# Performance work log

Hardware: AMD Instinct MI355X
Metric: run time of the kernel (lower is better)

## Reference

```python
import jax, jax.numpy as jnp
import numpy as np

NUM_HEADS = 16
NEG_INF = -9e15


def setup_inputs() -> dict:
    key = jax.random.key(0)
    k1, k2, k3 = jax.random.split(key, 3)
    B, S, D = 2, 2048, 1024
    # xavier-uniform-ish init scale for weights
    lim_qkv = float(np.sqrt(6.0 / (D + 3 * D)))
    lim_o = float(np.sqrt(6.0 / (D + D)))
    return {
        "x": jax.random.normal(k1, (B, S, D), dtype=jnp.float32),
        "w_qkv": jax.random.uniform(k2, (3 * D, D), minval=-lim_qkv, maxval=lim_qkv, dtype=jnp.float32),
        "b_qkv": jnp.zeros((3 * D,), dtype=jnp.float32),
        "w_o": jax.random.uniform(k3, (D, D), minval=-lim_o, maxval=lim_o, dtype=jnp.float32),
        "b_o": jnp.zeros((D,), dtype=jnp.float32),
    }


def reference(x, w_qkv, b_qkv, w_o, b_o):
    B, S, D = x.shape
    H = NUM_HEADS
    hd = D // H
    # qkv projection: [B,S,3D]
    qkv = x @ w_qkv.T + b_qkv
    # -> [B, H, S, 3*hd], then split
    qkv = qkv.reshape(B, S, H, 3 * hd).transpose(0, 2, 1, 3)
    q, k, v = jnp.split(qkv, 3, axis=-1)  # each [B,H,S,hd]
    scale = 1.0 / jnp.sqrt(jnp.asarray(hd, dtype=x.dtype))
    logits = jnp.einsum("bhqd,bhkd->bhqk", q, k) * scale
    attn = jax.nn.softmax(logits, axis=-1)
    vals = jnp.einsum("bhqk,bhkd->bhqd", attn, v)
    vals = vals.transpose(0, 2, 1, 3).reshape(B, S, D)
    return vals @ w_o.T + b_o
```

## Files before the change

### kernel.cpp

```cpp
#include <hip/hip_runtime.h>
#include <math.h>

#define NHEADS 16
#define HD 64

typedef __attribute__((ext_vector_type(8))) _Float16 half8;
typedef __attribute__((ext_vector_type(4))) _Float16 half4;
typedef __attribute__((ext_vector_type(4))) float f32x4;
typedef __attribute__((ext_vector_type(16))) float f32x16;
typedef __attribute__((ext_vector_type(4))) unsigned int u32x4;

__device__ inline void load_lds16(const void* g, void* l) {
    __builtin_amdgcn_global_load_lds(
        (const __attribute__((address_space(1))) unsigned int*)g,
        (__attribute__((address_space(3))) unsigned int*)l, 16, 0, 0);
}
__device__ inline void pl32swap(unsigned int& x, unsigned int& y) {
    asm volatile("v_permlane32_swap_b32 %0, %1" : "+v"(x), "+v"(y));
}

#define NX  4194304
#define NWQ 3145728
#define NWO 1048576
__global__ void cvt_all(const float* __restrict__ x, const float* __restrict__ wq,
                        const float* __restrict__ wo, _Float16* __restrict__ xf,
                        _Float16* __restrict__ wqf, _Float16* __restrict__ wof) {
    int i = (blockIdx.x * blockDim.x + threadIdx.x) * 8;
    const float* src; _Float16* dst; int off;
    if (i < NX)            { src = x;  dst = xf;  off = i; }
    else if (i < NX + NWQ) { src = wq; dst = wqf; off = i - NX; }
    else                   { src = wo; dst = wof; off = i - (NX + NWQ); }
    float4 a = *(const float4*)(src + off);
    float4 b = *(const float4*)(src + off + 4);
    half8 h;
    h[0] = (_Float16)a.x; h[1] = (_Float16)a.y; h[2] = (_Float16)a.z; h[3] = (_Float16)a.w;
    h[4] = (_Float16)b.x; h[5] = (_Float16)b.y; h[6] = (_Float16)b.z; h[7] = (_Float16)b.w;
    *(half8*)(dst + off) = h;
}

#define GEMM_SETUP(K, NTILE)                                                           \
    const int tid = threadIdx.x;                                                       \
    const int l = tid & 63, w = tid >> 6;                                              \
    const int wr = w >> 1, wc = w & 1;                                                 \
    const int nwg = gridDim.x * gridDim.y;                                             \
    const int bid = blockIdx.y * gridDim.x + blockIdx.x;                               \
    const int swz = (bid & 7) * (nwg >> 3) + (bid >> 3);                               \
    const int m0 = (swz / gridDim.x) * 128, n0 = (swz % gridDim.x) * (NTILE);          \
    const int srow = tid >> 2;                                                         \
    const int schunk = (tid & 3) ^ ((srow >> 1) & 3);                                  \
    const size_t gA0 = (size_t)(m0 + srow) * K + schunk * 8;                           \
    const size_t gA1 = gA0 + (size_t)64 * K;                                           \
    const size_t gB0 = (size_t)(n0 + srow) * K + schunk * 8;                           \
    unsigned char* ldsW = smem + w * 1024;                                             \
    const int col16 = l & 15, kc = l >> 4;                                             \
    const int ra0 = wr * 64 + col16;                                                   \
    const int offA = ra0 * 64 + ((kc ^ ((ra0 >> 1) & 3)) * 16);

#define QSCALE 0.18033688f
__global__ __launch_bounds__(256, 2) void gemm_qkv(
    const _Float16* __restrict__ A, const _Float16* __restrict__ B,
    const float* __restrict__ bias,
    _Float16* __restrict__ Qf, _Float16* __restrict__ Kf,
    _Float16* __restrict__ VfT, int K) {
    __shared__ __align__(1024) unsigned char smem[49152];
    GEMM_SETUP(K, 128)
    const size_t gB1 = gB0 + (size_t)64 * K;
    const int rb0 = wc * 64 + col16;
    const int offB = rb0 * 64 + ((kc ^ ((rb0 >> 1) & 3)) * 16);
    f32x4 acc[4][4] = {};

#define GSTAGE(k0_, buf_)                                                              \
    load_lds16(A + gA0 + (k0_), ldsW + (buf_) * 16384 + 0);                            \
    load_lds16(A + gA1 + (k0_), ldsW + (buf_) * 16384 + 4096);                         \
    load_lds16(B + gB0 + (k0_), ldsW + (buf_) * 16384 + 8192);                         \
    load_lds16(B + gB1 + (k0_), ldsW + (buf_) * 16384 + 12288);
#define GSTEP(s_, buf_, VM, dostage)                                                   \
    asm volatile("s_waitcnt " VM ::: "memory");                                        \
    __builtin_amdgcn_sched_barrier(0);                                                 \
    __builtin_amdgcn_s_barrier();                                                      \
    if (dostage) { GSTAGE(((s_) + 2) * 32, ((buf_) + 2) % 3) }                         \
    {                                                                                  \
        const unsigned char* bs = smem + (buf_) * 16384;                               \
        half8 af[4], bf[4];                                                            \
        _Pragma("unroll")                                                              \
        for (int m = 0; m < 4; ++m) af[m] = *(const half8*)(bs + offA + m * 1024);     \
        _Pragma("unroll")                                                              \
        for (int n = 0; n < 4; ++n) bf[n] = *(const half8*)(bs + 8192 + offB + n * 1024); \
        _Pragma("unroll")                                                              \
        for (int m = 0; m < 4; ++m)                                                    \
            _Pragma("unroll")                                                          \
            for (int n = 0; n < 4; ++n)                                                \
                acc[m][n] = __builtin_amdgcn_mfma_f32_16x16x32_f16(af[m], bf[n], acc[m][n], 0, 0, 0); \
    }

    GSTAGE(0, 0)
    GSTAGE(32, 1)
    for (int t = 0; t < 30; t += 3) {
        GSTEP(t, 0, "vmcnt(4)", 1)
        GSTEP(t + 1, 1, "vmcnt(4)", 1)
        GSTEP(t + 2, 2, "vmcnt(4)", 1)
    }
    GSTEP(30, 0, "vmcnt(4)", 0)
    GSTEP(31, 1, "vmcnt(0)", 0)
#undef GSTAGE
#undef GSTEP

    const int rowb = m0 + wr * 64 + (l >> 4) * 4;
    const int colb = n0 + wc * 64 + col16;
    #pragma unroll
    for (int n = 0; n < 4; ++n) {
        int col = colb + n * 16;
        int h = col / 192;
        int rem = col - h * 192;
        int part = rem >> 6, d = rem & 63;
        float bv = bias[col];
        #pragma unroll
        for (int m = 0; m < 4; ++m) {
            int r0 = rowb + m * 16;
            int b = r0 >> 11, s0r = r0 & 2047;
            int bh = b * 16 + h;
            if (part == 0) {
                #pragma unroll
                for (int j = 0; j < 4; ++j)
                    Qf[((size_t)bh * 2048 + s0r + j) * 64 + d] =
                        (_Float16)((acc[m][n][j] + bv) * QSCALE);
            } else if (part == 1) {
                #pragma unroll
                for (int j = 0; j < 4; ++j)
                    Kf[((size_t)bh * 2048 + s0r + j) * 64 + d] = (_Float16)(acc[m][n][j] + bv);
            } else {
                half4 pk;
                pk[0] = (_Float16)(acc[m][n][0] + bv);
                pk[1] = (_Float16)(acc[m][n][1] + bv);
                pk[2] = (_Float16)(acc[m][n][2] + bv);
                pk[3] = (_Float16)(acc[m][n][3] + bv);
                *(half4*)&VfT[((size_t)bh * 64 + d) * 2048 + s0r] = pk;
            }
        }
    }
}

__global__ __launch_bounds__(256, 2) void gemm_o(
    const _Float16* __restrict__ A, const _Float16* __restrict__ B,
    const float* __restrict__ bias, float* __restrict__ C,
    int M, int N, int K) {
    __shared__ __align__(1024) unsigned char smem[36864];
    GEMM_SETUP(K, 64)
    const int rb0 = wc * 32 + col16;
    const int offB = rb0 * 64 + ((kc ^ ((rb0 >> 1) & 3)) * 16);
    f32x4 acc[4][2] = {};

#define OSTAGE(k0_, buf_)                                                              \
    load_lds16(A + gA0 + (k0_), ldsW + (buf_) * 12288 + 0);                            \
    load_lds16(A + gA1 + (k0_), ldsW + (buf_) * 12288 + 4096);                         \
    load_lds16(B + gB0 + (k0_), ldsW + (buf_) * 12288 + 8192);
#define OSTEP(s_, buf_, VM, dostage)                                                   \
    asm volatile("s_waitcnt " VM ::: "memory");                                        \
    __builtin_amdgcn_sched_barrier(0);                                                 \
    __builtin_amdgcn_s_barrier();                                                      \
    if (dostage) { OSTAGE(((s_) + 2) * 32, ((buf_) + 2) % 3) }                         \
    {                                                                                  \
        const unsigned char* bs = smem + (buf_) * 12288;                               \
        half8 af[4], bf[2];                                                            \
        _Pragma("unroll")                                                              \
        for (int m = 0; m < 4; ++m) af[m] = *(const half8*)(bs + offA + m * 1024);     \
        _Pragma("unroll")                                                              \
        for (int n = 0; n < 2; ++n) bf[n] = *(const half8*)(bs + 8192 + offB + n * 1024); \
        _Pragma("unroll")                                                              \
        for (int m = 0; m < 4; ++m)                                                    \
            _Pragma("unroll")                                                          \
            for (int n = 0; n < 2; ++n)                                                \
                acc[m][n] = __builtin_amdgcn_mfma_f32_16x16x32_f16(af[m], bf[n], acc[m][n], 0, 0, 0); \
    }

    OSTAGE(0, 0)
    OSTAGE(32, 1)
    for (int t = 0; t < 30; t += 3) {
        OSTEP(t, 0, "vmcnt(3)", 1)
        OSTEP(t + 1, 1, "vmcnt(3)", 1)
        OSTEP(t + 2, 2, "vmcnt(3)", 1)
    }
    OSTEP(30, 0, "vmcnt(3)", 0)
    OSTEP(31, 1, "vmcnt(0)", 0)
#undef OSTAGE
#undef OSTEP

    const int rowb = m0 + wr * 64 + (l >> 4) * 4;
    const int colb = n0 + wc * 32 + col16;
    float bv[2];
    #pragma unroll
    for (int n = 0; n < 2; ++n) bv[n] = bias[colb + n * 16];
    #pragma unroll
    for (int m = 0; m < 4; ++m)
        #pragma unroll
        for (int j = 0; j < 4; ++j) {
            float* crow = C + (size_t)(rowb + m * 16 + j) * N + colb;
            #pragma unroll
            for (int n = 0; n < 2; ++n) crow[n * 16] = acc[m][n][j] + bv[n];
        }
}

__global__ __launch_bounds__(256, 2) void mfma_attn(
    const _Float16* __restrict__ Qf, const _Float16* __restrict__ Kf,
    const _Float16* __restrict__ VfT, _Float16* __restrict__ vals) {
    __shared__ __align__(1024) unsigned char smem[49152];
    const int tid = threadIdx.x;
    const int l = tid & 63, w = tid >> 6;
    const int l31 = l & 31, hl = l >> 5;
    const int hwbid = blockIdx.x;
    const int r_ = hwbid & 7;
    const int q_t = (hwbid >> 3) & 15;
    const int g_ = hwbid >> 7;
    const int bh = r_ + 8 * g_;
    const int q0 = q_t * 128;
    const int h = bh & 15, b = bh >> 4;

    half8 qf[4];
    {
        const _Float16* qp = Qf + ((size_t)bh * 2048 + q0 + w * 32 + l31) * 64 + hl * 8;
        #pragma unroll
        for (int c = 0; c < 4; ++c) qf[c] = *(const half8*)(qp + c * 16);
    }
    f32x16 zvec = {};
    f32x16 o0 = {}, o1 = {};
    float mshift = 0.f, lsum = 0.f;

    const _Float16* Kg = Kf + (size_t)bh * 2048 * 64;
    const _Float16* Vg = VfT + (size_t)bh * 64 * 2048;

    int offK[2], offV[2];
    #pragma unroll
    for (int i = 0; i < 2; ++i) {
        int row2 = w * 8 + i * 4 + (l >> 4);
        int slot = (l & 15) ^ (row2 & 15);
        int row = row2 * 2 + (slot >> 3);
        int chunk = slot & 7;
        offK[i] = row * 64 + chunk * 8;
        offV[i] = row * 2048 + chunk * 8;
    }
    const int sbase = (l31 & 1) * 8;
    const int xr = (l31 >> 1) & 15;
    const int rb0 = (l31 >> 1) * 256;

    #define STAGE(kt0, buf)                                                            \
        {                                                                              \
            unsigned char* bK = smem + (buf) * 16384 + w * 2048;                       \
            unsigned char* bV = bK + 8192;                                             \
            load_lds16(Kg + (size_t)(kt0) * 64 + offK[0], bK);                         \
            load_lds16(Kg + (size_t)(kt0) * 64 + offK[1], bK + 1024);                  \
            load_lds16(Vg + (kt0) + offV[0], bV);                                      \
            load_lds16(Vg + (kt0) + offV[1], bV + 1024);                               \
        }

    #define QK_TILE(slot_, D0, D1)                                                     \
        {                                                                              \
            const unsigned char* Ksb_ = smem + (slot_) * 16384;                        \
            {                                                                          \
                int chOff = ((sbase + hl) ^ xr) << 4;                                  \
                half8 k0_ = *(const half8*)(Ksb_ + rb0 + chOff);                       \
                half8 k1_ = *(const half8*)(Ksb_ + rb0 + 4096 + chOff);                \
                D0 = __builtin_amdgcn_mfma_f32_32x32x16_f16(k0_, qf[0], zvec, 0, 0, 0);\
                D1 = __builtin_amdgcn_mfma_f32_32x32x16_f16(k1_, qf[0], zvec, 0, 0, 0);\
            }                                                                          \
            _Pragma("unroll")                                                          \
            for (int kc = 1; kc < 4; ++kc) {                                           \
                int chOff = ((sbase + kc * 2 + hl) ^ xr) << 4;                         \
                half8 k0_ = *(const half8*)(Ksb_ + rb0 + chOff);                       \
                half8 k1_ = *(const half8*)(Ksb_ + rb0 + 4096 + chOff);                \
                D0 = __builtin_amdgcn_mfma_f32_32x32x16_f16(k0_, qf[kc], D0, 0, 0, 0); \
                D1 = __builtin_amdgcn_mfma_f32_32x32x16_f16(k1_, qf[kc], D1, 0, 0, 0); \
            }                                                                          \
        }

    #define SMPV(S0, S1, slot_)                                                        \
        {                                                                              \
            const unsigned char* Vsb_ = smem + (slot_) * 16384 + 8192;                 \
            if (__any(mshift != 0.f)) {                                                \
                _Pragma("unroll")                                                      \
                for (int r = 0; r < 16; ++r) { S0[r] -= mshift; S1[r] -= mshift; }     \
            }                                                                          \
            float r0 = 0.f, r1 = 0.f, r2 = 0.f, r3 = 0.f;                              \
            unsigned int a[2][8];                                                      \
            _Pragma("unroll")                                                          \
            for (int j = 0; j < 8; ++j) {                                              \
                float p0 = __builtin_amdgcn_exp2f(S0[2 * j]);                          \
                float p1 = __builtin_amdgcn_exp2f(S0[2 * j + 1]);                      \
                float q0_ = __builtin_amdgcn_exp2f(S1[2 * j]);                         \
                float q1_ = __builtin_amdgcn_exp2f(S1[2 * j + 1]);                     \
                r0 += p0; r1 += p1; r2 += q0_; r3 += q1_;                              \
                a[0][j] = __builtin_bit_cast(unsigned int, __builtin_amdgcn_cvt_pkrtz(p0, p1));   \
                a[1][j] = __builtin_bit_cast(unsigned int, __builtin_amdgcn_cvt_pkrtz(q0_, q1_)); \
            }                                                                          \
            float rsum = (r0 + r1) + (r2 + r3);                                        \
            if (__any(rsum > 32768.f)) {                                               \
                float pmax = S0[0];                                                    \
                _Pragma("unroll")                                                      \
                for (int r = 1; r < 16; ++r) pmax = fmaxf(pmax, S0[r]);                \
                _Pragma("unroll")                                                      \
                for (int r = 0; r < 16; ++r) pmax = fmaxf(pmax, S1[r]);                \
                pmax = fmaxf(pmax, __shfl_xor(pmax, 32, 64));                          \
                float d_ = fmaxf(pmax, 0.f);                                           \
                float corr = __builtin_amdgcn_exp2f(-d_);                              \
                _Pragma("unroll")                                                      \
                for (int r = 0; r < 16; ++r) { S0[r] -= d_; S1[r] -= d_; }             \
                _Pragma("unroll")                                                      \
                for (int r = 0; r < 16; ++r) { o0[r] *= corr; o1[r] *= corr; }         \
                lsum *= corr;                                                          \
                mshift += d_;                                                          \
                r0 = r1 = r2 = r3 = 0.f;                                               \
                _Pragma("unroll")                                                      \
                for (int j = 0; j < 8; ++j) {                                          \
                    float p0 = __builtin_amdgcn_exp2f(S0[2 * j]);                      \
                    float p1 = __builtin_amdgcn_exp2f(S0[2 * j + 1]);                  \
                    float q0_ = __builtin_amdgcn_exp2f(S1[2 * j]);                     \
                    float q1_ = __builtin_amdgcn_exp2f(S1[2 * j + 1]);                 \
                    r0 += p0; r1 += p1; r2 += q0_; r3 += q1_;                          \
                    a[0][j] = __builtin_bit_cast(unsigned int, __builtin_amdgcn_cvt_pkrtz(p0, p1));   \
                    a[1][j] = __builtin_bit_cast(unsigned int, __builtin_amdgcn_cvt_pkrtz(q0_, q1_)); \
                }                                                                      \
                rsum = (r0 + r1) + (r2 + r3);                                          \
            }                                                                          \
            lsum += rsum;                                                              \
            _Pragma("unroll")                                                          \
            for (int c = 0; c < 2; ++c) {                                              \
                pl32swap(a[c][0], a[c][2]);                                            \
                pl32swap(a[c][1], a[c][3]);                                            \
                pl32swap(a[c][4], a[c][6]);                                            \
                pl32swap(a[c][5], a[c][7]);                                            \
            }                                                                          \
            _Pragma("unroll")                                                          \
            for (int kk = 0; kk < 4; ++kk) {                                           \
                u32x4 pw;                                                              \
                pw.x = a[kk >> 1][(kk & 1) * 4 + 0];                                   \
                pw.y = a[kk >> 1][(kk & 1) * 4 + 1];                                   \
                pw.z = a[kk >> 1][(kk & 1) * 4 + 2];                                   \
                pw.w = a[kk >> 1][(kk & 1) * 4 + 3];                                   \
                half8 pf = __builtin_bit_cast(half8, pw);                              \
                int chOff = ((sbase + kk * 2 + hl) ^ xr) << 4;                         \
                half8 v0 = *(const half8*)(Vsb_ + rb0 + chOff);                        \
                half8 v1 = *(const half8*)(Vsb_ + rb0 + 4096 + chOff);                 \
                o0 = __builtin_amdgcn_mfma_f32_32x32x16_f16(v0, pf, o0, 0, 0, 0);      \
                o1 = __builtin_amdgcn_mfma_f32_32x32x16_f16(v1, pf, o1, 0, 0, 0);      \
            }                                                                          \
        }

    #define AITER(tt, kb, VM, dostage)                                                 \
        asm volatile("s_waitcnt " VM ::: "memory");                                    \
        __builtin_amdgcn_sched_barrier(0);                                             \
        __builtin_amdgcn_s_barrier();                                                  \
        if (dostage) STAGE(((tt) + 2) * 64, ((kb) + 2) % 3)                            \
        QK_TILE(kb, sS0, sS1)                                                          \
        SMPV(sS0, sS1, kb)

    STAGE(0, 0)
    STAGE(64, 1)
    f32x16 sS0, sS1;
    for (int t = 0; t < 30; t += 3) {
        AITER(t, 0, "vmcnt(4)", 1)
        AITER(t + 1, 1, "vmcnt(4)", 1)
        AITER(t + 2, 2, "vmcnt(4)", 1)
    }
    AITER(30, 0, "vmcnt(4)", 0)
    AITER(31, 1, "vmcnt(0)", 0)

    lsum += __shfl_xor(lsum, 32, 64);
    float inv = 1.f / lsum;
    size_t orow = ((size_t)(b * 2048 + q0 + w * 32 + l31)) * 1024 + h * 64;
    #pragma unroll
    for (int dc = 0; dc < 2; ++dc) {
        const f32x16* op = dc ? &o1 : &o0;
        #pragma unroll
        for (int rq = 0; rq < 4; ++rq) {
            int d0 = dc * 32 + rq * 8 + hl * 4;
            half4 hv;
            #pragma unroll
            for (int j = 0; j < 4; ++j) hv[j] = (_Float16)((*op)[rq * 4 + j] * inv);
            *(half4*)(vals + orow + d0) = hv;
        }
    }
}

extern "C" void kernel_launch(void* const* d_in, const int* in_sizes, int n_in,
                              void* d_out, int out_size, void* d_ws, size_t ws_size,
                              hipStream_t stream) {
    const float* x     = (const float*)d_in[0];
    const float* w_qkv = (const float*)d_in[1];
    const float* b_qkv = (const float*)d_in[2];
    const float* w_o   = (const float*)d_in[3];
    const float* b_o   = (const float*)d_in[4];
    float* out = (float*)d_out;

    const int B = 2, S = 2048, D = 1024;
    const int M = B * S;
    const int N1 = 3 * D;
    const int BH = B * NHEADS;

    _Float16* xf  = (_Float16*)d_ws;
    _Float16* wqf = xf  + (size_t)M * D;
    _Float16* wof = wqf + (size_t)N1 * D;
    _Float16* Qf  = wof + (size_t)D * D;
    _Float16* Kf  = Qf  + (size_t)BH * S * HD;
    _Float16* VfT = Kf  + (size_t)BH * S * HD;
    _Float16* vals = xf;

    cvt_all<<<(NX + NWQ + NWO) / 2048, 256, 0, stream>>>(x, w_qkv, w_o, xf, wqf, wof);

    gemm_qkv<<<dim3(N1 / 128, M / 128), 256, 0, stream>>>(xf, wqf, b_qkv, Qf, Kf, VfT, D);

    mfma_attn<<<dim3(512), 256, 0, stream>>>(Qf, Kf, VfT, vals);

    gemm_o<<<dim3(D / 64, M / 128), 256, 0, stream>>>(vals, wof, b_o, out, M, D, D);
}
```

Measured before the change: 109.8 us.

## Split attention KV range across two wave groups, each wave handling 64 query rows

The attention kernel now launches 256 blocks of 512 threads, each covering 256 query rows. Each wave processes two 32-row query tiles against shared K/V fragments, so every LDS K/V read feeds twice as many MFMAs. The two halves of the block each take alternate KV tiles, which is a split-K over the key sequence. Their partial softmax states are merged through LDS at the end. This doubles register pressure and LDS per block, leaves fewer blocks than before, and adds a final reduction and barrier.

```diff
diff --git a/kernel.cpp b/kernel.cpp
--- a/kernel.cpp
+++ b/kernel.cpp
@@ -200,30 +200,32 @@
         }
 }
 
-__global__ __launch_bounds__(256, 2) void mfma_attn(
+__global__ __launch_bounds__(512, 2) void mfma_attn(
     const _Float16* __restrict__ Qf, const _Float16* __restrict__ Kf,
     const _Float16* __restrict__ VfT, _Float16* __restrict__ vals) {
-    __shared__ __align__(1024) unsigned char smem[49152];
+    __shared__ __align__(1024) unsigned char smem[98304];
     const int tid = threadIdx.x;
     const int l = tid & 63, w = tid >> 6;
+    const int wq = w & 3, hh = w >> 2;
     const int l31 = l & 31, hl = l >> 5;
     const int hwbid = blockIdx.x;
-    const int r_ = hwbid & 7;
-    const int q_t = (hwbid >> 3) & 15;
-    const int g_ = hwbid >> 7;
-    const int bh = r_ + 8 * g_;
-    const int q0 = q_t * 128;
+    const int q_t = (hwbid >> 3) & 7;
+    const int bh = (hwbid & 7) + ((hwbid >> 6) << 3);
+    const int q0 = q_t * 256;
     const int h = bh & 15, b = bh >> 4;
 
-    half8 qf[4];
+    half8 qfA[4], qfB[4];
     {
-        const _Float16* qp = Qf + ((size_t)bh * 2048 + q0 + w * 32 + l31) * 64 + hl * 8;
-        #pragma unroll
-        for (int c = 0; c < 4; ++c) qf[c] = *(const half8*)(qp + c * 16);
+        const _Float16* qp = Qf + ((size_t)bh * 2048 + q0 + wq * 64 + l31) * 64 + hl * 8;
+        #pragma unroll
+        for (int c = 0; c < 4; ++c) qfA[c] = *(const half8*)(qp + c * 16);
+        qp += (size_t)32 * 64;
+        #pragma unroll
+        for (int c = 0; c < 4; ++c) qfB[c] = *(const half8*)(qp + c * 16);
     }
     f32x16 zvec = {};
-    f32x16 o0 = {}, o1 = {};
-    float mshift = 0.f, lsum = 0.f;
+    f32x16 oA0 = {}, oA1 = {}, oB0 = {}, oB1 = {};
+    float msA = 0.f, msB = 0.f, lsA = 0.f, lsB = 0.f;
 
     const _Float16* Kg = Kf + (size_t)bh * 2048 * 64;
     const _Float16* Vg = VfT + (size_t)bh * 64 * 2048;
@@ -231,7 +233,7 @@
     int offK[2], offV[2];
     #pragma unroll
     for (int i = 0; i < 2; ++i) {
-        int row2 = w * 8 + i * 4 + (l >> 4);
+        int row2 = wq * 8 + i * 4 + (l >> 4);
         int slot = (l & 15) ^ (row2 & 15);
         int row = row2 * 2 + (slot >> 3);
         int chunk = slot & 7;
@@ -242,45 +244,48 @@
     const int xr = (l31 >> 1) & 15;
     const int rb0 = (l31 >> 1) * 256;
 
-    #define STAGE(kt0, buf)                                                            \
+    #define STAGE(it_, slot_)                                                          \
         {                                                                              \
-            unsigned char* bK = smem + (buf) * 16384 + w * 2048;                       \
+            int kt0_ = (((it_) * 2 + hh)) * 64;                                        \
+            unsigned char* bK = smem + hh * 49152 + (slot_) * 16384 + wq * 2048;       \
             unsigned char* bV = bK + 8192;                                             \
-            load_lds16(Kg + (size_t)(kt0) * 64 + offK[0], bK);                         \
-            load_lds16(Kg + (size_t)(kt0) * 64 + offK[1], bK + 1024);                  \
-            load_lds16(Vg + (kt0) + offV[0], bV);                                      \
-            load_lds16(Vg + (kt0) + offV[1], bV + 1024);                               \
-        }
-
-    #define QK_TILE(slot_, D0, D1)                                                     \
+            load_lds16(Kg + (size_t)kt0_ * 64 + offK[0], bK);                          \
+            load_lds16(Kg + (size_t)kt0_ * 64 + offK[1], bK + 1024);                   \
+            load_lds16(Vg + kt0_ + offV[0], bV);                                       \
+            load_lds16(Vg + kt0_ + offV[1], bV + 1024);                                \
+        }
+
+    #define QK2(slot_)                                                                 \
         {                                                                              \
-            const unsigned char* Ksb_ = smem + (slot_) * 16384;                        \
+            const unsigned char* Ksb_ = smem + hh * 49152 + (slot_) * 16384;           \
             {                                                                          \
                 int chOff = ((sbase + hl) ^ xr) << 4;                                  \
                 half8 k0_ = *(const half8*)(Ksb_ + rb0 + chOff);                       \
                 half8 k1_ = *(const half8*)(Ksb_ + rb0 + 4096 + chOff);                \
-                D0 = __builtin_amdgcn_mfma_f32_32x32x16_f16(k0_, qf[0], zvec, 0, 0, 0);\
-                D1 = __builtin_amdgcn_mfma_f32_32x32x16_f16(k1_, qf[0], zvec, 0, 0, 0);\
+                sA0 = __builtin_amdgcn_mfma_f32_32x32x16_f16(k0_, qfA[0], zvec, 0, 0, 0); \
+                sA1 = __builtin_amdgcn_mfma_f32_32x32x16_f16(k1_, qfA[0], zvec, 0, 0, 0); \
+                sB0 = __builtin_amdgcn_mfma_f32_32x32x16_f16(k0_, qfB[0], zvec, 0, 0, 0); \
+                sB1 = __builtin_amdgcn_mfma_f32_32x32x16_f16(k1_, qfB[0], zvec, 0, 0, 0); \
             }                                                                          \
             _Pragma("unroll")                                                          \
             for (int kc = 1; kc < 4; ++kc) {                                           \
                 int chOff = ((sbase + kc * 2 + hl) ^ xr) << 4;                         \
                 half8 k0_ = *(const half8*)(Ksb_ + rb0 + chOff);                       \
                 half8 k1_ = *(const half8*)(Ksb_ + rb0 + 4096 + chOff);                \
-                D0 = __builtin_amdgcn_mfma_f32_32x32x16_f16(k0_, qf[kc], D0, 0, 0, 0); \
-                D1 = __builtin_amdgcn_mfma_f32_32x32x16_f16(k1_, qf[kc], D1, 0, 0, 0); \
-            }                                                                          \
-        }
-
-    #define SMPV(S0, S1, slot_)                                                        \
+                sA0 = __builtin_amdgcn_mfma_f32_32x32x16_f16(k0_, qfA[kc], sA0, 0, 0, 0); \
+                sA1 = __builtin_amdgcn_mfma_f32_32x32x16_f16(k1_, qfA[kc], sA1, 0, 0, 0); \
+                sB0 = __builtin_amdgcn_mfma_f32_32x32x16_f16(k0_, qfB[kc], sB0, 0, 0, 0); \
+                sB1 = __builtin_amdgcn_mfma_f32_32x32x16_f16(k1_, qfB[kc], sB1, 0, 0, 0); \
+            }                                                                          \
+        }
+
+    #define SM_G(S0, S1, O0, O1, AA, ls_, ms_)                                         \
         {                                                                              \
-            const unsigned char* Vsb_ = smem + (slot_) * 16384 + 8192;                 \
-            if (__any(mshift != 0.f)) {                                                \
-                _Pragma("unroll")                                                      \
-                for (int r = 0; r < 16; ++r) { S0[r] -= mshift; S1[r] -= mshift; }     \
+            if (__any(ms_ != 0.f)) {                                                   \
+                _Pragma("unroll")                                                      \
+                for (int r = 0; r < 16; ++r) { S0[r] -= ms_; S1[r] -= ms_; }           \
             }                                                                          \
             float r0 = 0.f, r1 = 0.f, r2 = 0.f, r3 = 0.f;                              \
-            unsigned int a[2][8];                                                      \
             _Pragma("unroll")                                                          \
             for (int j = 0; j < 8; ++j) {                                              \
                 float p0 = __builtin_amdgcn_exp2f(S0[2 * j]);                          \
@@ -288,8 +293,8 @@
                 float q0_ = __builtin_amdgcn_exp2f(S1[2 * j]);                         \
                 float q1_ = __builtin_amdgcn_exp2f(S1[2 * j + 1]);                     \
                 r0 += p0; r1 += p1; r2 += q0_; r3 += q1_;                              \
-                a[0][j] = __builtin_bit_cast(unsigned int, __builtin_amdgcn_cvt_pkrtz(p0, p1));   \
-                a[1][j] = __builtin_bit_cast(unsigned int, __builtin_amdgcn_cvt_pkrtz(q0_, q1_)); \
+                AA[0][j] = __builtin_bit_cast(unsigned int, __builtin_amdgcn_cvt_pkrtz(p0, p1));   \
+                AA[1][j] = __builtin_bit_cast(unsigned int, __builtin_amdgcn_cvt_pkrtz(q0_, q1_)); \
             }                                                                          \
             float rsum = (r0 + r1) + (r2 + r3);                                        \
             if (__any(rsum > 32768.f)) {                                               \
@@ -304,9 +309,9 @@
                 _Pragma("unroll")                                                      \
                 for (int r = 0; r < 16; ++r) { S0[r] -= d_; S1[r] -= d_; }             \
                 _Pragma("unroll")                                                      \
-                for (int r = 0; r < 16; ++r) { o0[r] *= corr; o1[r] *= corr; }         \
-                lsum *= corr;                                                          \
-                mshift += d_;                                                          \
+                for (int r = 0; r < 16; ++r) { O0[r] *= corr; O1[r] *= corr; }         \
+                ls_ *= corr;                                                           \
+                ms_ += d_;                                                             \
                 r0 = r1 = r2 = r3 = 0.f;                                               \
                 _Pragma("unroll")                                                      \
                 for (int j = 0; j < 8; ++j) {                                          \
@@ -315,67 +320,128 @@
                     float q0_ = __builtin_amdgcn_exp2f(S1[2 * j]);                     \
                     float q1_ = __builtin_amdgcn_exp2f(S1[2 * j + 1]);                 \
                     r0 += p0; r1 += p1; r2 += q0_; r3 += q1_;                          \
-                    a[0][j] = __builtin_bit_cast(unsigned int, __builtin_amdgcn_cvt_pkrtz(p0, p1));   \
-                    a[1][j] = __builtin_bit_cast(unsigned int, __builtin_amdgcn_cvt_pkrtz(q0_, q1_)); \
+                    AA[0][j] = __builtin_bit_cast(unsigned int, __builtin_amdgcn_cvt_pkrtz(p0, p1));   \
+                    AA[1][j] = __builtin_bit_cast(unsigned int, __builtin_amdgcn_cvt_pkrtz(q0_, q1_)); \
                 }                                                                      \
                 rsum = (r0 + r1) + (r2 + r3);                                          \
             }                                                                          \
-            lsum += rsum;                                                              \
+            ls_ += rsum;                                                               \
             _Pragma("unroll")                                                          \
             for (int c = 0; c < 2; ++c) {                                              \
-                pl32swap(a[c][0], a[c][2]);                                            \
-                pl32swap(a[c][1], a[c][3]);                                            \
-                pl32swap(a[c][4], a[c][6]);                                            \
-                pl32swap(a[c][5], a[c][7]);                                            \
-            }                                                                          \
+                pl32swap(AA[c][0], AA[c][2]);                                          \
+                pl32swap(AA[c][1], AA[c][3]);                                          \
+                pl32swap(AA[c][4], AA[c][6]);                                          \
+                pl32swap(AA[c][5], AA[c][7]);                                          \
+            }                                                                          \
+        }
+
+    #define PV2(slot_)                                                                 \
+        {                                                                              \
+            const unsigned char* Vsb_ = smem + hh * 49152 + (slot_) * 16384 + 8192;    \
             _Pragma("unroll")                                                          \
             for (int kk = 0; kk < 4; ++kk) {                                           \
-                u32x4 pw;                                                              \
-                pw.x = a[kk >> 1][(kk & 1) * 4 + 0];                                   \
-                pw.y = a[kk >> 1][(kk & 1) * 4 + 1];                                   \
-                pw.z = a[kk >> 1][(kk & 1) * 4 + 2];                                   \
-                pw.w = a[kk >> 1][(kk & 1) * 4 + 3];                                   \
-                half8 pf = __builtin_bit_cast(half8, pw);                              \
+                u32x4 pwA, pwB;                                                        \
+                pwA.x = aA[kk >> 1][(kk & 1) * 4 + 0];                                 \
+                pwA.y = aA[kk >> 1][(kk & 1) * 4 + 1];                                 \
+                pwA.z = aA[kk >> 1][(kk & 1) * 4 + 2];                                 \
+                pwA.w = aA[kk >> 1][(kk & 1) * 4 + 3];                                 \
+                pwB.x = aB[kk >> 1][(kk & 1) * 4 + 0];                                 \
+                pwB.y = aB[kk >> 1][(kk & 1) * 4 + 1];                                 \
+                pwB.z = aB[kk >> 1][(kk & 1) * 4 + 2];                                 \
+                pwB.w = aB[kk >> 1][(kk & 1) * 4 + 3];                                 \
+                half8 pfA = __builtin_bit_cast(half8, pwA);                            \
+                half8 pfB = __builtin_bit_cast(half8, pwB);                            \
                 int chOff = ((sbase + kk * 2 + hl) ^ xr) << 4;                         \
                 half8 v0 = *(const half8*)(Vsb_ + rb0 + chOff);                        \
                 half8 v1 = *(const half8*)(Vsb_ + rb0 + 4096 + chOff);                 \
-                o0 = __builtin_amdgcn_mfma_f32_32x32x16_f16(v0, pf, o0, 0, 0, 0);      \
-                o1 = __builtin_amdgcn_mfma_f32_32x32x16_f16(v1, pf, o1, 0, 0, 0);      \
-            }                                                                          \
-        }
-
-    #define AITER(tt, kb, VM, dostage)                                                 \
+                oA0 = __builtin_amdgcn_mfma_f32_32x32x16_f16(v0, pfA, oA0, 0, 0, 0);   \
+                oA1 = __builtin_amdgcn_mfma_f32_32x32x16_f16(v1, pfA, oA1, 0, 0, 0);   \
+                oB0 = __builtin_amdgcn_mfma_f32_32x32x16_f16(v0, pfB, oB0, 0, 0, 0);   \
+                oB1 = __builtin_amdgcn_mfma_f32_32x32x16_f16(v1, pfB, oB1, 0, 0, 0);   \
+            }                                                                          \
+        }
+
+    #define AITER(tt, slot_, VM, dostage)                                              \
         asm volatile("s_waitcnt " VM ::: "memory");                                    \
         __builtin_amdgcn_sched_barrier(0);                                             \
         __builtin_amdgcn_s_barrier();                                                  \
-        if (dostage) STAGE(((tt) + 2) * 64, ((kb) + 2) % 3)                            \
-        QK_TILE(kb, sS0, sS1)                                                          \
-        SMPV(sS0, sS1, kb)
+        if (dostage) STAGE((tt) + 2, ((slot_) + 2) % 3)                                \
+        QK2(slot_)                                                                     \
+        {                                                                              \
+            unsigned int aA[2][8], aB[2][8];                                           \
+            SM_G(sA0, sA1, oA0, oA1, aA, lsA, msA)                                     \
+            SM_G(sB0, sB1, oB0, oB1, aB, lsB, msB)                                     \
+            PV2(slot_)                                                                 \
+        }
 
     STAGE(0, 0)
-    STAGE(64, 1)
-    f32x16 sS0, sS1;
-    for (int t = 0; t < 30; t += 3) {
-        AITER(t, 0, "vmcnt(4)", 1)
-        AITER(t + 1, 1, "vmcnt(4)", 1)
-        AITER(t + 2, 2, "vmcnt(4)", 1)
-    }
-    AITER(30, 0, "vmcnt(4)", 0)
-    AITER(31, 1, "vmcnt(0)", 0)
-
-    lsum += __shfl_xor(lsum, 32, 64);
-    float inv = 1.f / lsum;
-    size_t orow = ((size_t)(b * 2048 + q0 + w * 32 + l31)) * 1024 + h * 64;
-    #pragma unroll
-    for (int dc = 0; dc < 2; ++dc) {
-        const f32x16* op = dc ? &o1 : &o0;
-        #pragma unroll
-        for (int rq = 0; rq < 4; ++rq) {
-            int d0 = dc * 32 + rq * 8 + hl * 4;
-            half4 hv;
+    STAGE(1, 1)
+    f32x16 sA0, sA1, sB0, sB1;
+    for (int p = 0; p < 12; p += 3) {
+        AITER(p, 0, "vmcnt(4)", 1)
+        AITER(p + 1, 1, "vmcnt(4)", 1)
+        AITER(p + 2, 2, "vmcnt(4)", 1)
+    }
+    AITER(12, 0, "vmcnt(4)", 1)
+    AITER(13, 1, "vmcnt(4)", 1)
+    AITER(14, 2, "vmcnt(4)", 0)
+    AITER(15, 0, "vmcnt(0)", 0)
+
+    lsA += __shfl_xor(lsA, 32, 64);
+    lsB += __shfl_xor(lsB, 32, 64);
+
+    __syncthreads();
+    float* mb = (float*)smem;
+    const int mybase = (wq * 64 + l) * 68;
+    if (hh == 1) {
+        #pragma unroll
+        for (int r = 0; r < 16; ++r) {
+            mb[mybase + r]      = oA0[r];
+            mb[mybase + 16 + r] = oA1[r];
+            mb[mybase + 32 + r] = oB0[r];
+            mb[mybase + 48 + r] = oB1[r];
+        }
+        mb[mybase + 64] = lsA;
+        mb[mybase + 65] = lsB;
+        mb[mybase + 66] = msA;
+        mb[mybase + 67] = msB;
+    }
+    __syncthreads();
+    if (hh == 0) {
+        float l1A = mb[mybase + 64], l1B = mb[mybase + 65];
+        float m1A = mb[mybase + 66], m1B = mb[mybase + 67];
+        float MA = fmaxf(msA, m1A);
+        float fA0 = __builtin_amdgcn_exp2f(msA - MA), fA1 = __builtin_amdgcn_exp2f(m1A - MA);
+        float MB = fmaxf(msB, m1B);
+        float fB0 = __builtin_amdgcn_exp2f(msB - MB), fB1 = __builtin_amdgcn_exp2f(m1B - MB);
+        lsA = lsA * fA0 + l1A * fA1;
+        lsB = lsB * fB0 + l1B * fB1;
+        #pragma unroll
+        for (int r = 0; r < 16; ++r) {
+            oA0[r] = oA0[r] * fA0 + mb[mybase + r] * fA1;
+            oA1[r] = oA1[r] * fA0 + mb[mybase + 16 + r] * fA1;
+            oB0[r] = oB0[r] * fB0 + mb[mybase + 32 + r] * fB1;
+            oB1[r] = oB1[r] * fB0 + mb[mybase + 48 + r] * fB1;
+        }
+        float invA = 1.f / lsA, invB = 1.f / lsB;
+        size_t orowA = ((size_t)(b * 2048 + q0 + wq * 64 + l31)) * 1024 + h * 64;
+        size_t orowB = orowA + (size_t)32 * 1024;
+        #pragma unroll
+        for (int dc = 0; dc < 2; ++dc) {
+            const f32x16* opA = dc ? &oA1 : &oA0;
+            const f32x16* opB = dc ? &oB1 : &oB0;
             #pragma unroll
-            for (int j = 0; j < 4; ++j) hv[j] = (_Float16)((*op)[rq * 4 + j] * inv);
-            *(half4*)(vals + orow + d0) = hv;
+            for (int rq = 0; rq < 4; ++rq) {
+                int d0 = dc * 32 + rq * 8 + hl * 4;
+                half4 hvA, hvB;
+                #pragma unroll
+                for (int j = 0; j < 4; ++j) {
+                    hvA[j] = (_Float16)((*opA)[rq * 4 + j] * invA);
+                    hvB[j] = (_Float16)((*opB)[rq * 4 + j] * invB);
+                }
+                *(half4*)(vals + orowA + d0) = hvA;
+                *(half4*)(vals + orowB + d0) = hvB;
+            }
         }
     }
 }
@@ -407,7 +473,7 @@
 
     gemm_qkv<<<dim3(N1 / 128, M / 128), 256, 0, stream>>>(xf, wqf, b_qkv, Qf, Kf, VfT, D);
 
-    mfma_attn<<<dim3(512), 256, 0, stream>>>(Qf, Kf, VfT, vals);
+    mfma_attn<<<dim3(256), 512, 0, stream>>>(Qf, Kf, VfT, vals);
 
     gemm_o<<<dim3(D / 64, M / 128), 256, 0, stream>>>(vals, wof, b_o, out, M, D, D);
 }
```

Measured after the change: 108.9 us. About the same (-0.9%).
